# Kernel tuning notes

Hardware: AMD Instinct MI355X
Metric: run time of the kernel (lower is better)

## Reference

```python
import jax, jax.numpy as jnp
import numpy as np

B = 1024      # batch of videos
T = 32768     # max snippets per video


def setup_inputs() -> dict:
    key = jax.random.key(0)
    k1, k2, k3 = jax.random.split(key, 3)
    # sigmoid-like scores in (0,1) as BCELoss expects probabilities
    scores = jax.random.uniform(k1, (B, T), dtype=jnp.float32, minval=1e-4, maxval=1.0 - 1e-4)
    label = jax.random.uniform(k2, (B,), dtype=jnp.float32)
    seqlen = jax.random.randint(k3, (B,), 1, T + 1, dtype=jnp.int32)
    return {"scores": scores, "label": label, "seqlen": seqlen}


def reference(scores, label, seqlen):
    # fwd_topk with cfg.k == -1: per-sample k_i = seqlen_i // 16 + 1,
    # mean of the top-k_i scores within the valid prefix scores[i, :seqlen_i],
    # followed by BCELoss against label.
    _, t = scores.shape
    pos = jnp.arange(t)[None, :]                      # [1, T]
    valid = pos < seqlen[:, None]                     # [B, T] ragged-length mask
    # push invalid tail to -inf so descending sort puts valid values first
    masked = jnp.where(valid, scores, -jnp.inf)
    srt = -jnp.sort(-masked, axis=1)                  # descending sort, valid prefix first
    # zero out the (-inf) tail; exactly seqlen_i leading entries are valid
    srt = jnp.where(valid, srt, 0.0)
    csum = jnp.cumsum(srt, axis=1)                    # prefix sums of sorted scores
    k = seqlen // 16 + 1                              # per-sample k, always <= seqlen
    topk_sum = jnp.take_along_axis(csum, (k - 1)[:, None], axis=1)[:, 0]
    vl_scores = topk_sum / k.astype(scores.dtype)     # mean of top-k per sample, [B]
    # BCELoss (mean reduction)
    loss = -jnp.mean(label * jnp.log(vl_scores) + (1.0 - label) * jnp.log1p(-vl_scores))
    return loss
```

## Files before the change

### kernel.cpp

```cpp
#include <hip/hip_runtime.h>
#include <math.h>

#define NB   4096
#define BLK  256
#define CHW  (NB / BLK)
#define CAP  2048

__global__ void zero_out_kernel(float* __restrict__ out) {
    out[0] = 0.0f;
}

__global__ __launch_bounds__(BLK) void topk_bce_kernel(
    const float* __restrict__ scores,
    const float* __restrict__ label,
    const int*   __restrict__ seqlen,
    float*       __restrict__ out,
    int T, int B)
{
    __shared__ int   cnt[NB];
    __shared__ float buf[CAP];
    __shared__ int   schunk[BLK];
    __shared__ float wsum[BLK / 64];
    __shared__ int   s_b, s_r, s_above, s_ccount;

    const int row = blockIdx.x;
    const int tid = threadIdx.x;
    const int n   = seqlen[row];
    const int k   = (n >> 4) + 1;
    const float* rp  = scores + (size_t)row * (size_t)T;
    const float4* rp4 = (const float4*)rp;
    const int n4 = n >> 2;
    const float scale = (float)NB;

#define BIN(x) min(NB - 1, (int)((x) * scale))

    for (int i = tid; i < NB; i += BLK) cnt[i] = 0;
    if (tid == 0) s_ccount = 0;
    __syncthreads();

    for (int j = tid; j < n4; j += BLK) {
        float4 v = rp4[j];
        atomicAdd(&cnt[BIN(v.x)], 1);
        atomicAdd(&cnt[BIN(v.y)], 1);
        atomicAdd(&cnt[BIN(v.z)], 1);
        atomicAdd(&cnt[BIN(v.w)], 1);
    }
    for (int j = (n4 << 2) + tid; j < n; j += BLK) {
        atomicAdd(&cnt[BIN(rp[j])], 1);
    }
    __syncthreads();

    {
        int c = 0;
        const int base = tid * CHW;
        #pragma unroll
        for (int j = 0; j < CHW; ++j) c += cnt[base + j];
        schunk[tid] = c;
    }
    __syncthreads();

    for (int off = 1; off < BLK; off <<= 1) {
        int v = schunk[tid];
        if (tid + off < BLK) v += schunk[tid + off];
        __syncthreads();
        schunk[tid] = v;
        __syncthreads();
    }

    {
        int SA     = schunk[tid];
        int SAnext = (tid + 1 < BLK) ? schunk[tid + 1] : 0;
        if (SA >= k && SAnext < k) {
            s_above = SAnext;
            s_b     = tid;
        }
    }
    __syncthreads();

    if (tid == 0) {
        const int t   = s_b;
        int acc = s_above;
        int b = t * CHW, r = k - acc;
        for (int j = CHW - 1; j >= 0; --j) {
            const int bin = t * CHW + j;
            const int cb  = cnt[bin];
            if (acc + cb >= k) { b = bin; r = k - acc; break; }
            acc += cb;
        }
        s_b = b; s_r = r;
    }
    __syncthreads();
    const int b = s_b;
    const int r = s_r;

    float lsum = 0.f;
#define PROC(x) do { \
        const float _x = (x); \
        const int _bn = BIN(_x); \
        if (_bn > b) lsum += _x; \
        else if (_bn == b) { \
            int p = atomicAdd(&s_ccount, 1); \
            if (p < CAP) buf[p] = _x; \
        } \
    } while (0)

    for (int j = tid; j < n4; j += BLK) {
        float4 v = rp4[j];
        PROC(v.x); PROC(v.y); PROC(v.z); PROC(v.w);
    }
    for (int j = (n4 << 2) + tid; j < n; j += BLK) PROC(rp[j]);
#undef PROC

    for (int off = 32; off > 0; off >>= 1) lsum += __shfl_down(lsum, off, 64);
    if ((tid & 63) == 0) wsum[tid >> 6] = lsum;
    __syncthreads();

    if (tid == 0) {
        float above_sum = wsum[0] + wsum[1] + wsum[2] + wsum[3];
        const int m  = s_ccount;
        const int mm = min(m, CAP);
        const int rr = min(r, mm);
        float top = 0.f;
        for (int s = 0; s < rr; ++s) {
            float best = -1.f; int bi = 0;
            for (int j = 0; j < mm; ++j) {
                const float x = buf[j];
                if (x > best) { best = x; bi = j; }
            }
            top += best;
            buf[bi] = -1.f;
        }
        if (r > rr) {
            top += (float)(r - rr) * ((float)(b) + 0.5f) * (1.0f / NB);
        }
        float v = (above_sum + top) / (float)k;
        v = fminf(fmaxf(v, 1e-12f), 1.0f - 1e-7f);
        const float lab  = label[row];
        const float loss = -(lab * logf(v) + (1.0f - lab) * log1pf(-v));
        atomicAdd(out, loss / (float)B);
    }
#undef BIN
}

extern "C" void kernel_launch(void* const* d_in, const int* in_sizes, int n_in,
                              void* d_out, int out_size, void* d_ws, size_t ws_size,
                              hipStream_t stream) {
    const float* scores = (const float*)d_in[0];
    const float* label  = (const float*)d_in[1];
    const int*   seqlen = (const int*)d_in[2];
    float* out = (float*)d_out;

    const int B = in_sizes[1];
    const int T = in_sizes[0] / B;

    zero_out_kernel<<<1, 1, 0, stream>>>(out);
    topk_bce_kernel<<<B, BLK, 0, stream>>>(scores, label, seqlen, out, T, B);
}
```

Baseline: 211.3 us.

## Split per-row top-k into multi-block segmented histogram, select, collect and final kernels

Splits the single one-block-per-row kernel into five kernels. Each row is cut into 8192-element segments processed by separate blocks, which merge their partial histograms and sums through global atomics. The histogram shrinks from 4096 to 512 bins, and the serial single-thread selection of boundary-bin values becomes a wave-parallel argmax in a 64-thread final kernel. This raises parallelism for long rows and removes the serial tail. In exchange it adds launches, workspace traffic and global atomics, and coarser bins put more candidates in the boundary bin, which is capped at 1024 entries before falling back to an approximation.

```diff
diff --git a/kernel.cpp b/kernel.cpp
--- a/kernel.cpp
+++ b/kernel.cpp
@@ -1,64 +1,82 @@
 #include <hip/hip_runtime.h>
 #include <math.h>
 
-#define NB   4096
+#define NB   512
+#define CAP  1024
+#define SEG  8192
 #define BLK  256
-#define CHW  (NB / BLK)
-#define CAP  2048
-
-__global__ void zero_out_kernel(float* __restrict__ out) {
-    out[0] = 0.0f;
-}
-
-__global__ __launch_bounds__(BLK) void topk_bce_kernel(
-    const float* __restrict__ scores,
-    const float* __restrict__ label,
-    const int*   __restrict__ seqlen,
-    float*       __restrict__ out,
-    int T, int B)
-{
-    __shared__ int   cnt[NB];
-    __shared__ float buf[CAP];
-    __shared__ int   schunk[BLK];
-    __shared__ float wsum[BLK / 64];
-    __shared__ int   s_b, s_r, s_above, s_ccount;
+
+__device__ __forceinline__ int bin_of(float x) {
+    int b = (int)(x * (float)NB);
+    return b > NB - 1 ? NB - 1 : b;
+}
+
+__global__ void zero_kernel(int* __restrict__ ghist, float* __restrict__ rowsum,
+                            int* __restrict__ bufcnt, float* __restrict__ out,
+                            int nh, int B) {
+    const int i = blockIdx.x * blockDim.x + threadIdx.x;
+    if (i < nh) ghist[i] = 0;
+    if (i < B) { rowsum[i] = 0.f; bufcnt[i] = 0; }
+    if (i == 0) out[0] = 0.f;
+}
+
+__global__ __launch_bounds__(BLK) void hist_kernel(
+    const float* __restrict__ scores, const int* __restrict__ seqlen,
+    int* __restrict__ ghist, int T, int nseg)
+{
+    const int gid = blockIdx.x;
+    const int row = gid / nseg;
+    const int seg = gid - row * nseg;
+    const int n   = seqlen[row];
+    const int s0  = seg * SEG;
+    int cn = n - s0;
+    if (cn <= 0) return;
+    if (cn > SEG) cn = SEG;
+
+    __shared__ int h[NB];
+    for (int i = threadIdx.x; i < NB; i += BLK) h[i] = 0;
+    __syncthreads();
+
+    const float*  rp  = scores + (size_t)row * (size_t)T + s0;
+    const float4* rp4 = (const float4*)rp;
+    const int n4 = cn >> 2;
+    for (int j = threadIdx.x; j < n4; j += BLK) {
+        float4 v = rp4[j];
+        atomicAdd(&h[bin_of(v.x)], 1);
+        atomicAdd(&h[bin_of(v.y)], 1);
+        atomicAdd(&h[bin_of(v.z)], 1);
+        atomicAdd(&h[bin_of(v.w)], 1);
+    }
+    for (int j = (n4 << 2) + threadIdx.x; j < cn; j += BLK)
+        atomicAdd(&h[bin_of(rp[j])], 1);
+    __syncthreads();
+
+    int* gh = ghist + (size_t)row * NB;
+    for (int i = threadIdx.x; i < NB; i += BLK) {
+        const int c = h[i];
+        if (c) atomicAdd(&gh[i], c);
+    }
+}
+
+__global__ __launch_bounds__(BLK) void select_kernel(
+    const int* __restrict__ ghist, const int* __restrict__ seqlen,
+    int2* __restrict__ brs)
+{
+    __shared__ int c[NB];
+    __shared__ int schunk[BLK];
+    __shared__ int s_t, s_above;
 
     const int row = blockIdx.x;
     const int tid = threadIdx.x;
     const int n   = seqlen[row];
     const int k   = (n >> 4) + 1;
-    const float* rp  = scores + (size_t)row * (size_t)T;
-    const float4* rp4 = (const float4*)rp;
-    const int n4 = n >> 2;
-    const float scale = (float)NB;
-
-#define BIN(x) min(NB - 1, (int)((x) * scale))
-
-    for (int i = tid; i < NB; i += BLK) cnt[i] = 0;
-    if (tid == 0) s_ccount = 0;
-    __syncthreads();
-
-    for (int j = tid; j < n4; j += BLK) {
-        float4 v = rp4[j];
-        atomicAdd(&cnt[BIN(v.x)], 1);
-        atomicAdd(&cnt[BIN(v.y)], 1);
-        atomicAdd(&cnt[BIN(v.z)], 1);
-        atomicAdd(&cnt[BIN(v.w)], 1);
-    }
-    for (int j = (n4 << 2) + tid; j < n; j += BLK) {
-        atomicAdd(&cnt[BIN(rp[j])], 1);
-    }
-    __syncthreads();
-
-    {
-        int c = 0;
-        const int base = tid * CHW;
-        #pragma unroll
-        for (int j = 0; j < CHW; ++j) c += cnt[base + j];
-        schunk[tid] = c;
-    }
-    __syncthreads();
-
+    const int* gh = ghist + (size_t)row * NB;
+
+    for (int i = tid; i < NB; i += BLK) c[i] = gh[i];
+    __syncthreads();
+
+    schunk[tid] = c[2 * tid] + c[2 * tid + 1];
+    __syncthreads();
     for (int off = 1; off < BLK; off <<= 1) {
         int v = schunk[tid];
         if (tid + off < BLK) v += schunk[tid + off];
@@ -66,80 +84,125 @@
         schunk[tid] = v;
         __syncthreads();
     }
-
     {
-        int SA     = schunk[tid];
-        int SAnext = (tid + 1 < BLK) ? schunk[tid + 1] : 0;
-        if (SA >= k && SAnext < k) {
-            s_above = SAnext;
-            s_b     = tid;
-        }
+        const int SA  = schunk[tid];
+        const int SAn = (tid + 1 < BLK) ? schunk[tid + 1] : 0;
+        if (SA >= k && SAn < k) { s_t = tid; s_above = SAn; }
     }
     __syncthreads();
 
     if (tid == 0) {
-        const int t   = s_b;
-        int acc = s_above;
-        int b = t * CHW, r = k - acc;
-        for (int j = CHW - 1; j >= 0; --j) {
-            const int bin = t * CHW + j;
-            const int cb  = cnt[bin];
-            if (acc + cb >= k) { b = bin; r = k - acc; break; }
-            acc += cb;
-        }
-        s_b = b; s_r = r;
-    }
-    __syncthreads();
-    const int b = s_b;
-    const int r = s_r;
+        const int t     = s_t;
+        const int above = s_above;
+        int b, r;
+        const int c_hi = c[2 * t + 1];
+        if (above + c_hi >= k) { b = 2 * t + 1; r = k - above; }
+        else                   { b = 2 * t;     r = k - above - c_hi; }
+        brs[row] = make_int2(b, r);
+    }
+}
+
+__global__ __launch_bounds__(BLK) void collect_kernel(
+    const float* __restrict__ scores, const int* __restrict__ seqlen,
+    const int2* __restrict__ brs, float* __restrict__ rowsum,
+    int* __restrict__ bufcnt, float* __restrict__ bbuf, int T, int nseg)
+{
+    const int gid = blockIdx.x;
+    const int row = gid / nseg;
+    const int seg = gid - row * nseg;
+    const int n   = seqlen[row];
+    const int s0  = seg * SEG;
+    int cn = n - s0;
+    if (cn <= 0) return;
+    if (cn > SEG) cn = SEG;
+
+    const int b = brs[row].x;
+    const float*  rp  = scores + (size_t)row * (size_t)T + s0;
+    const float4* rp4 = (const float4*)rp;
+    float* bb = bbuf + (size_t)row * CAP;
+    int*   bc = bufcnt + row;
 
     float lsum = 0.f;
 #define PROC(x) do { \
         const float _x = (x); \
-        const int _bn = BIN(_x); \
+        const int _bn = bin_of(_x); \
         if (_bn > b) lsum += _x; \
         else if (_bn == b) { \
-            int p = atomicAdd(&s_ccount, 1); \
-            if (p < CAP) buf[p] = _x; \
+            int p = atomicAdd(bc, 1); \
+            if (p < CAP) bb[p] = _x; \
         } \
     } while (0)
 
-    for (int j = tid; j < n4; j += BLK) {
+    const int n4 = cn >> 2;
+    for (int j = threadIdx.x; j < n4; j += BLK) {
         float4 v = rp4[j];
         PROC(v.x); PROC(v.y); PROC(v.z); PROC(v.w);
     }
-    for (int j = (n4 << 2) + tid; j < n; j += BLK) PROC(rp[j]);
+    for (int j = (n4 << 2) + threadIdx.x; j < cn; j += BLK) PROC(rp[j]);
 #undef PROC
 
+    __shared__ float wsum[BLK / 64];
     for (int off = 32; off > 0; off >>= 1) lsum += __shfl_down(lsum, off, 64);
-    if ((tid & 63) == 0) wsum[tid >> 6] = lsum;
-    __syncthreads();
-
-    if (tid == 0) {
-        float above_sum = wsum[0] + wsum[1] + wsum[2] + wsum[3];
-        const int m  = s_ccount;
-        const int mm = min(m, CAP);
-        const int rr = min(r, mm);
-        float top = 0.f;
-        for (int s = 0; s < rr; ++s) {
-            float best = -1.f; int bi = 0;
-            for (int j = 0; j < mm; ++j) {
-                const float x = buf[j];
-                if (x > best) { best = x; bi = j; }
-            }
-            top += best;
-            buf[bi] = -1.f;
+    if ((threadIdx.x & 63) == 0) wsum[threadIdx.x >> 6] = lsum;
+    __syncthreads();
+    if (threadIdx.x == 0)
+        atomicAdd(&rowsum[row], wsum[0] + wsum[1] + wsum[2] + wsum[3]);
+}
+
+__global__ __launch_bounds__(64) void final_kernel(
+    const float* __restrict__ label, const int* __restrict__ seqlen,
+    const int2* __restrict__ brs, const float* __restrict__ rowsum,
+    const int* __restrict__ bufcnt, const float* __restrict__ bbuf,
+    float* __restrict__ out, int B)
+{
+    const int row  = blockIdx.x;
+    const int lane = threadIdx.x;
+    const int n    = seqlen[row];
+    const int k    = (n >> 4) + 1;
+    const int2 br  = brs[row];
+    const int r0   = br.y;
+    int m = bufcnt[row]; if (m > CAP) m = CAP;
+    const int rr = r0 < m ? r0 : m;
+    const float* bb = bbuf + (size_t)row * CAP;
+
+    float local[CAP / 64];
+    #pragma unroll
+    for (int j = 0; j < CAP / 64; ++j) {
+        const int idx = lane + 64 * j;
+        local[j] = (idx < m) ? bb[idx] : -1.f;
+    }
+
+    float tot = 0.f;
+    for (int s = 0; s < rr; ++s) {
+        float lm = -1.f; int li = 0;
+        #pragma unroll
+        for (int j = 0; j < CAP / 64; ++j)
+            if (local[j] > lm) { lm = local[j]; li = j; }
+        float wm = lm;
+        #pragma unroll
+        for (int off = 32; off > 0; off >>= 1)
+            wm = fmaxf(wm, __shfl_down(wm, off, 64));
+        wm = __shfl(wm, 0, 64);
+        const unsigned long long ball = __ballot(lm == wm);
+        const int owner = (int)__ffsll(ball) - 1;
+        if (lane == owner) {
+            #pragma unroll
+            for (int j = 0; j < CAP / 64; ++j)
+                if (j == li) local[j] = -1.f;
         }
-        if (r > rr) {
-            top += (float)(r - rr) * ((float)(b) + 0.5f) * (1.0f / NB);
-        }
-        float v = (above_sum + top) / (float)k;
-        v = fminf(fmaxf(v, 1e-12f), 1.0f - 1e-7f);
+        tot += wm;
+    }
+
+    if (lane == 0) {
+        float top = tot;
+        if (r0 > rr)
+            top += (float)(r0 - rr) * (((float)br.x + 0.5f) / (float)NB);
+        float v = (rowsum[row] + top) / (float)k;
+        v = fminf(fmaxf(v, 1e-12f), 1.f - 1e-7f);
         const float lab  = label[row];
-        const float loss = -(lab * logf(v) + (1.0f - lab) * log1pf(-v));
+        const float loss = -(lab * logf(v) + (1.f - lab) * log1pf(-v));
         atomicAdd(out, loss / (float)B);
     }
-#undef BIN
 }
 
 extern "C" void kernel_launch(void* const* d_in, const int* in_sizes, int n_in,
@@ -152,7 +215,20 @@
 
     const int B = in_sizes[1];
     const int T = in_sizes[0] / B;
-
-    zero_out_kernel<<<1, 1, 0, stream>>>(out);
-    topk_bce_kernel<<<B, BLK, 0, stream>>>(scores, label, seqlen, out, T, B);
-}
+    const int nseg = (T + SEG - 1) / SEG;
+
+    char* ws = (char*)d_ws;
+    int*   ghist  = (int*)ws;
+    float* rowsum = (float*)(ws + (size_t)B * NB * 4);
+    int*   bufcnt = (int*)  (ws + (size_t)B * NB * 4 + (size_t)B * 4);
+    int2*  brs    = (int2*) (ws + (size_t)B * NB * 4 + (size_t)B * 8);
+    float* bbuf   = (float*)(ws + (size_t)B * NB * 4 + (size_t)B * 16);
+
+    const int nh = B * NB;
+    const int zmax = nh > B ? nh : B;
+    zero_kernel<<<(zmax + 255) / 256, 256, 0, stream>>>(ghist, rowsum, bufcnt, out, nh, B);
+    hist_kernel<<<B * nseg, BLK, 0, stream>>>(scores, seqlen, ghist, T, nseg);
+    select_kernel<<<B, BLK, 0, stream>>>(ghist, seqlen, brs);
+    collect_kernel<<<B * nseg, BLK, 0, stream>>>(scores, seqlen, brs, rowsum, bufcnt, bbuf, T, nseg);
+    final_kernel<<<B, 64, 0, stream>>>(label, seqlen, brs, rowsum, bufcnt, bbuf, out, B);
+}
```

Result: slower. 249.7 us (+18.2%).
